# Optimization experiments

Hardware: AMD Instinct MI355X
Metric: run time of the kernel (lower is better)

Reference implementation:

```python
import jax, jax.numpy as jnp
import numpy as np

N_NODES = 100000
N_EDGES = 625000
D = 128
N_LAYERS = 10

def setup_inputs() -> dict:
    key = jax.random.key(0)
    ks = jax.random.split(key, 6)
    x = jax.random.normal(ks[0], (N_NODES, D), dtype=jnp.float32)
    edge_index = jax.random.randint(ks[1], (2, N_EDGES), 0, N_NODES, dtype=jnp.int32)
    # PyG SAGEConv params per layer: lin_l (aggregated msgs, with bias), lin_r (root, no bias)
    scale = 1.0 / np.sqrt(D)
    Wl = jax.random.normal(ks[2], (N_LAYERS, D, D), dtype=jnp.float32) * scale
    Wr = jax.random.normal(ks[3], (N_LAYERS, D, D), dtype=jnp.float32) * scale
    b = jax.random.normal(ks[4], (N_LAYERS, D), dtype=jnp.float32) * 0.01
    return {"x": x, "Wl": Wl, "Wr": Wr, "b": b, "edge_index": edge_index}

def reference(x, Wl, Wr, b, edge_index):
    src = edge_index[0]
    dst = edge_index[1]
    n = x.shape[0]
    # in-degree for mean aggregation (clamped to avoid div by zero)
    deg = jax.ops.segment_sum(jnp.ones(src.shape[0], x.dtype), dst, num_segments=n)
    deg = jnp.maximum(deg, 1.0)[:, None]
    n_layers = Wl.shape[0]
    for i in range(n_layers):
        # SAGEConv: out = lin_l(mean_{j in N(i)} x_j) + lin_r(x_i)
        agg = jax.ops.segment_sum(x[src], dst, num_segments=n) / deg
        x = agg @ Wl[i] + x @ Wr[i] + b[i]
        if i < n_layers - 1:
            x = jax.nn.relu(x)  # dropout is identity in eval mode
    return x
```

## Files before the change

kernel.cpp:

```cpp
#include <hip/hip_runtime.h>
#include <hip/hip_bf16.h>

#define N_NODES 100000
#define N_EDGES 625000
#define D 128
#define N_LAYERS 10
#define SCAN_BLOCKS 98

typedef __attribute__((ext_vector_type(8))) short bf16x8;
typedef __attribute__((ext_vector_type(4))) float floatx4;

static __device__ __forceinline__ ushort f2bf(float f) {
    uint u = __float_as_uint(f);
    u += 0x7fff + ((u >> 16) & 1);
    return (ushort)(u >> 16);
}
static __device__ __forceinline__ float bf2f(ushort h) {
    return __uint_as_float(((uint)h) << 16);
}


__global__ void hist_kernel(const int* __restrict__ dst, int* __restrict__ deg) {
    int e = blockIdx.x * blockDim.x + threadIdx.x;
    if (e < N_EDGES) atomicAdd(&deg[dst[e]], 1);
}

__global__ void scanA_kernel(const int* __restrict__ deg, int* __restrict__ offsets,
                             int* __restrict__ blockSums) {
    __shared__ int s[1024];
    int tid = threadIdx.x;
    int i = blockIdx.x * 1024 + tid;
    int v = (i < N_NODES) ? deg[i] : 0;
    s[tid] = v;
    __syncthreads();
    for (int d = 1; d < 1024; d <<= 1) {
        int t = (tid >= d) ? s[tid - d] : 0;
        __syncthreads();
        s[tid] += t;
        __syncthreads();
    }
    if (i < N_NODES) offsets[i] = s[tid] - v;
    if (tid == 1023) blockSums[blockIdx.x] = s[1023];
}

__global__ void scanB_kernel(const int* __restrict__ blockSums, int* __restrict__ blockOffsets) {
    __shared__ int s[128];
    int tid = threadIdx.x;
    int v = (tid < SCAN_BLOCKS) ? blockSums[tid] : 0;
    s[tid] = v;
    __syncthreads();
    for (int d = 1; d < 128; d <<= 1) {
        int t = (tid >= d) ? s[tid - d] : 0;
        __syncthreads();
        s[tid] += t;
        __syncthreads();
    }
    blockOffsets[tid] = s[tid] - v;
}

__global__ void scanC_kernel(int* __restrict__ offsets, const int* __restrict__ blockOffsets) {
    int i = blockIdx.x * 1024 + threadIdx.x;
    if (i < N_NODES) offsets[i] += blockOffsets[blockIdx.x];
}

__global__ void invdeg_kernel(const int* __restrict__ deg, float* __restrict__ invdeg) {
    int i = blockIdx.x * blockDim.x + threadIdx.x;
    if (i < N_NODES) {
        int d = deg[i];
        invdeg[i] = 1.0f / (float)(d > 0 ? d : 1);
    }
}

__global__ void scatter_kernel(const int* __restrict__ src, const int* __restrict__ dst,
                               const int* __restrict__ offsets, int* __restrict__ fill,
                               int* __restrict__ srcSorted) {
    int e = blockIdx.x * blockDim.x + threadIdx.x;
    if (e < N_EDGES) {
        int d_ = dst[e];
        int pos = offsets[d_] + atomicAdd(&fill[d_], 1);
        srcSorted[pos] = src[e];
    }
}

__global__ void wsplit_kernel(const float* __restrict__ Wl, const float* __restrict__ Wr,
                              ushort* __restrict__ Whi, ushort* __restrict__ Wlo) {
    int t = blockIdx.x * blockDim.x + threadIdx.x;
    if (t >= N_LAYERS * 4 * 16 * 64) return;
    int lane  = t & 63;
    int ntile = (t >> 6) & 15;
    int s     = (t >> 10) & 3;
    int layer = t >> 12;
    int n = ntile * 16 + (lane & 15);
    int kbase = s * 32 + (lane >> 4) * 8;
    const float* W = (n < 128) ? (Wl + (size_t)layer * D * D + n)
                               : (Wr + (size_t)layer * D * D + (n - 128));
    size_t off = (size_t)t * 8;
#pragma unroll
    for (int j = 0; j < 8; ++j) {
        float w = W[(size_t)(kbase + j) * D];
        ushort hh = f2bf(w);
        Whi[off + j] = hh;
        Wlo[off + j] = f2bf(w - bf2f(hh));
    }
}

__global__ __launch_bounds__(256) void gemm_hz(
        const float* __restrict__ X, const ushort* __restrict__ Whi,
        const ushort* __restrict__ Wlo, const float* __restrict__ bias,
        uint* __restrict__ h2out, float* __restrict__ z) {
    __shared__ ushort Ahi[2][4 * 64 * 8];
    __shared__ ushort Alo[2][4 * 64 * 8];

    int tid  = threadIdx.x;
    int lane = tid & 63;
    int wave = tid >> 6;

    int r    = tid >> 4;
    int t0   = tid & 15;
    int s_st = t0 >> 2;
    int q_st = t0 & 3;
    int lanep = (q_st << 4) | r;
    int stIdx = (s_st * 64 + (lanep ^ (s_st << 2))) * 8;

    int q  = lane >> 4;
    int cc = lane & 15;

    int ntileMap[4];
#pragma unroll
    for (int nt = 0; nt < 4; ++nt)
        ntileMap[nt] = (wave < 2) ? (wave * 2 + (nt & 1) + ((nt >> 1) << 2))
                                  : (wave * 4 + nt);

    float bsc[4] = {0.f, 0.f, 0.f, 0.f};
    if (wave >= 2) {
#pragma unroll
        for (int nt = 0; nt < 4; ++nt)
            bsc[nt] = bias[((wave * 4 + nt) - 8) * 16 + cc];
    }

    for (int mt = blockIdx.x; mt < N_NODES / 32; mt += gridDim.x) {
        int row0 = mt * 32;
#pragma unroll
        for (int st = 0; st < 2; ++st) {
            const float* xp = X + (size_t)(row0 + st * 16 + r) * D + t0 * 8;
            float4 v0 = *(const float4*)xp;
            float4 v1 = *(const float4*)(xp + 4);
            float a[8] = {v0.x, v0.y, v0.z, v0.w, v1.x, v1.y, v1.z, v1.w};
            ushort hi8[8], lo8[8];
#pragma unroll
            for (int j = 0; j < 8; ++j) {
                ushort hh = f2bf(a[j]);
                hi8[j] = hh;
                lo8[j] = f2bf(a[j] - bf2f(hh));
            }
            *(bf16x8*)&Ahi[st][stIdx] = *(bf16x8*)hi8;
            *(bf16x8*)&Alo[st][stIdx] = *(bf16x8*)lo8;
        }
        __syncthreads();

        floatx4 acc0[4], acc1[4];
#pragma unroll
        for (int nt = 0; nt < 4; ++nt) {
            acc0[nt] = (floatx4){0.f, 0.f, 0.f, 0.f};
            acc1[nt] = (floatx4){0.f, 0.f, 0.f, 0.f};
        }
#pragma unroll
        for (int s = 0; s < 4; ++s) {
            int aIdx = (s * 64 + (lane ^ (s << 2))) * 8;
            bf16x8 ah0 = *(const bf16x8*)&Ahi[0][aIdx];
            bf16x8 al0 = *(const bf16x8*)&Alo[0][aIdx];
            bf16x8 ah1 = *(const bf16x8*)&Ahi[1][aIdx];
            bf16x8 al1 = *(const bf16x8*)&Alo[1][aIdx];
#pragma unroll
            for (int nt = 0; nt < 4; ++nt) {
                size_t wo = ((size_t)(s * 16 + ntileMap[nt]) * 64 + lane) * 8;
                bf16x8 wh = *(const bf16x8*)&Whi[wo];
                bf16x8 wl = *(const bf16x8*)&Wlo[wo];
                acc0[nt] = __builtin_amdgcn_mfma_f32_16x16x32_bf16(ah0, wh, acc0[nt], 0, 0, 0);
                acc0[nt] = __builtin_amdgcn_mfma_f32_16x16x32_bf16(al0, wh, acc0[nt], 0, 0, 0);
                acc0[nt] = __builtin_amdgcn_mfma_f32_16x16x32_bf16(ah0, wl, acc0[nt], 0, 0, 0);
                acc1[nt] = __builtin_amdgcn_mfma_f32_16x16x32_bf16(ah1, wh, acc1[nt], 0, 0, 0);
                acc1[nt] = __builtin_amdgcn_mfma_f32_16x16x32_bf16(al1, wh, acc1[nt], 0, 0, 0);
                acc1[nt] = __builtin_amdgcn_mfma_f32_16x16x32_bf16(ah1, wl, acc1[nt], 0, 0, 0);
            }
        }
        __syncthreads();

#pragma unroll
        for (int st = 0; st < 2; ++st) {
            floatx4* acc = st ? acc1 : acc0;
            int rowb = row0 + st * 16;
            if (wave < 2) {
#pragma unroll
                for (int p = 0; p < 2; ++p) {
                    int c = wave * 32 + p * 16 + cc;
#pragma unroll
                    for (int rr = 0; rr < 4; ++rr) {
                        uint lo = f2bf(acc[p][rr]);
                        uint hi = f2bf(acc[p + 2][rr]);
                        h2out[(size_t)(rowb + q * 4 + rr) * 64 + c] = lo | (hi << 16);
                    }
                }
            } else {
#pragma unroll
                for (int nt = 0; nt < 4; ++nt) {
                    int col = ((wave * 4 + nt) - 8) * 16 + cc;
#pragma unroll
                    for (int rr = 0; rr < 4; ++rr) {
                        int row = rowb + q * 4 + rr;
                        z[(size_t)row * D + col] = acc[nt][rr] + bsc[nt];
                    }
                }
            }
        }
    }
}

__global__ __launch_bounds__(256) void agg_add_kernel(
        const uint* __restrict__ h2, const int* __restrict__ srcSorted,
        const int* __restrict__ offsets, const int* __restrict__ deg,
        const float* __restrict__ invdeg, const float* __restrict__ zin,
        float* __restrict__ out, int relu) {
    int node = blockIdx.x * 4 + (threadIdx.x >> 6);
    int lane = threadIdx.x & 63;
    int off = offsets[node];
    int cnt = deg[node];
    float sx = 0.f, sy = 0.f;
    if (cnt > 0) {
        int nv = cnt < 64 ? cnt : 64;
        int idxv = srcSorted[off + ((lane < nv) ? lane : 0)];
        for (int k = 0; k < nv; k += 8) {
            int sidx[8];
#pragma unroll
            for (int j = 0; j < 8; ++j) {
                int kk = k + j;
                sidx[j] = __shfl(idxv, (kk < nv) ? kk : 0, 64);
            }
            uint u[8];
#pragma unroll
            for (int j = 0; j < 8; ++j)
                u[j] = h2[(size_t)sidx[j] * 64 + lane];
#pragma unroll
            for (int j = 0; j < 8; ++j) {
                float m = ((k + j) < nv) ? 1.f : 0.f;
                sx += m * __uint_as_float(u[j] << 16);
                sy += m * __uint_as_float(u[j] & 0xffff0000u);
            }
        }
        for (int k = 64; k < cnt; ++k) {
            int s = srcSorted[off + k];
            uint u = h2[(size_t)s * 64 + lane];
            sx += __uint_as_float(u << 16);
            sy += __uint_as_float(u & 0xffff0000u);
        }
    }
    float inv = invdeg[node];
    float ox = sx * inv + zin[(size_t)node * 128 + lane];
    float oy = sy * inv + zin[(size_t)node * 128 + 64 + lane];
    if (relu) { ox = fmaxf(ox, 0.f); oy = fmaxf(oy, 0.f); }
    out[(size_t)node * 128 + lane] = ox;
    out[(size_t)node * 128 + 64 + lane] = oy;
}

extern "C" void kernel_launch(void* const* d_in, const int* in_sizes, int n_in,
                              void* d_out, int out_size, void* d_ws, size_t ws_size,
                              hipStream_t stream) {
    const float* x  = (const float*)d_in[0];
    const float* Wl = (const float*)d_in[1];
    const float* Wr = (const float*)d_in[2];
    const float* b  = (const float*)d_in[3];
    const int*   ei = (const int*)d_in[4];
    const int* src = ei;
    const int* dst = ei + N_EDGES;
    float* out = (float*)d_out;

    char* w = (char*)d_ws;
    auto alloc = [&](size_t bytes) -> char* {
        char* p = w;
        w += (bytes + 255) & ~(size_t)255;
        return p;
    };
    float*  zx        = (float*)alloc((size_t)N_NODES * D * 4);
    uint*   hbuf      = (uint*)alloc((size_t)N_NODES * 64 * 4);
    ushort* Whi       = (ushort*)alloc((size_t)N_LAYERS * 4 * 16 * 64 * 8 * 2);
    ushort* Wlo       = (ushort*)alloc((size_t)N_LAYERS * 4 * 16 * 64 * 8 * 2);
    int*    deg       = (int*)alloc((size_t)N_NODES * 4);
    int*    offsets   = (int*)alloc((size_t)N_NODES * 4);
    int*    fill      = (int*)alloc((size_t)N_NODES * 4);
    int*    srcSorted = (int*)alloc((size_t)N_EDGES * 4);
    int*    blockSums = (int*)alloc(128 * 4);
    int*    blockOffs = (int*)alloc(128 * 4);
    float*  invdeg    = (float*)alloc((size_t)N_NODES * 4);

    hipMemsetAsync(deg, 0, (size_t)N_NODES * 4, stream);
    hipMemsetAsync(fill, 0, (size_t)N_NODES * 4, stream);

    hist_kernel<<<(N_EDGES + 255) / 256, 256, 0, stream>>>(dst, deg);
    scanA_kernel<<<SCAN_BLOCKS, 1024, 0, stream>>>(deg, offsets, blockSums);
    scanB_kernel<<<1, 128, 0, stream>>>(blockSums, blockOffs);
    scanC_kernel<<<SCAN_BLOCKS, 1024, 0, stream>>>(offsets, blockOffs);
    invdeg_kernel<<<(N_NODES + 255) / 256, 256, 0, stream>>>(deg, invdeg);
    scatter_kernel<<<(N_EDGES + 255) / 256, 256, 0, stream>>>(src, dst, offsets, fill, srcSorted);
    wsplit_kernel<<<(N_LAYERS * 4 * 16 * 64 + 255) / 256, 256, 0, stream>>>(Wl, Wr, Whi, Wlo);

    const float* cur = x;
    for (int L = 0; L < N_LAYERS; ++L) {
        size_t woff = (size_t)L * 4 * 16 * 64 * 8;
        gemm_hz<<<N_NODES / 32, 256, 0, stream>>>(cur, Whi + woff, Wlo + woff,
                                                  b + (size_t)L * D, hbuf, zx);
        float* o = (L == N_LAYERS - 1) ? out : zx;
        agg_add_kernel<<<N_NODES / 4, 256, 0, stream>>>(
            hbuf, srcSorted, offsets, deg, invdeg, zx, o, (L < N_LAYERS - 1) ? 1 : 0);
        cur = o;
    }
}
```

Baseline: 884.4 us.

## Fuse aggregation with next layer's GEMM into a single per-layer kernel

Each middle layer now runs one kernel that gathers neighbour messages for 32 nodes, adds the root/bias term and applies ReLU, then writes the bf16 hi/lo split straight into shared memory and runs the MFMA GEMM for the next layer. This removes the fp32 activation round trip to global memory and one launch per layer, and double-buffers the packed message buffer so reads and writes do not alias. The gather path uses a shared index load per wave covering 8 nodes. The trade-off is more register and LDS pressure, and each GEMM block now waits on irregular gather latency.

```diff
diff --git a/kernel.cpp b/kernel.cpp
--- a/kernel.cpp
+++ b/kernel.cpp
@@ -63,12 +63,14 @@
     if (i < N_NODES) offsets[i] += blockOffsets[blockIdx.x];
 }
 
-__global__ void invdeg_kernel(const int* __restrict__ deg, float* __restrict__ invdeg) {
+__global__ void invdeg_kernel(const int* __restrict__ deg, float* __restrict__ invdeg,
+                              int* __restrict__ offsets) {
     int i = blockIdx.x * blockDim.x + threadIdx.x;
     if (i < N_NODES) {
         int d = deg[i];
         invdeg[i] = 1.0f / (float)(d > 0 ? d : 1);
     }
+    if (i == 0) offsets[N_NODES] = N_EDGES;
 }
 
 __global__ void scatter_kernel(const int* __restrict__ src, const int* __restrict__ dst,
@@ -138,7 +140,8 @@
             bsc[nt] = bias[((wave * 4 + nt) - 8) * 16 + cc];
     }
 
-    for (int mt = blockIdx.x; mt < N_NODES / 32; mt += gridDim.x) {
+    int mt = blockIdx.x;
+    {
         int row0 = mt * 32;
 #pragma unroll
         for (int st = 0; st < 2; ++st) {
@@ -184,7 +187,6 @@
                 acc1[nt] = __builtin_amdgcn_mfma_f32_16x16x32_bf16(ah1, wl, acc1[nt], 0, 0, 0);
             }
         }
-        __syncthreads();
 
 #pragma unroll
         for (int st = 0; st < 2; ++st) {
@@ -216,11 +218,183 @@
     }
 }
 
+__global__ __launch_bounds__(256) void fused_layer(
+        const uint* __restrict__ h2in, const int* __restrict__ srcSorted,
+        const int* __restrict__ offsets, const float* __restrict__ invdeg,
+        const float* __restrict__ zio, const ushort* __restrict__ Whi,
+        const ushort* __restrict__ Wlo, const float* __restrict__ bias,
+        uint* __restrict__ h2out) {
+    __shared__ ushort Ahi[2][4 * 64 * 8];
+    __shared__ ushort Alo[2][4 * 64 * 8];
+
+    int tid  = threadIdx.x;
+    int lane = tid & 63;
+    int wave = tid >> 6;
+    int row0 = blockIdx.x * 32;
+
+    int n0 = row0 + wave * 8;
+    int offA[9];
+#pragma unroll
+    for (int i = 0; i < 9; ++i) offA[i] = offsets[n0 + i];
+    int off0 = offA[0];
+    int total = offA[8] - off0;
+    int idxv = srcSorted[min(off0 + ((lane < total) ? lane : 0), N_EDGES - 1)];
+
+    for (int i = 0; i < 8; ++i) {
+        int sRel = offA[i] - off0;
+        int eRel = offA[i + 1] - off0;
+        int cnt = eRel - sRel;
+        float sx = 0.f, sy = 0.f;
+        if (cnt > 0 && eRel <= 64) {
+            for (int k = sRel; k < eRel; k += 8) {
+                int sidx[8];
+#pragma unroll
+                for (int j = 0; j < 8; ++j) {
+                    int kk = k + j;
+                    sidx[j] = __shfl(idxv, (kk < eRel) ? kk : sRel, 64);
+                }
+                uint u[8];
+#pragma unroll
+                for (int j = 0; j < 8; ++j)
+                    u[j] = h2in[(size_t)sidx[j] * 64 + lane];
+#pragma unroll
+                for (int j = 0; j < 8; ++j) {
+                    float m = ((k + j) < eRel) ? 1.f : 0.f;
+                    sx += m * __uint_as_float(u[j] << 16);
+                    sy += m * __uint_as_float(u[j] & 0xffff0000u);
+                }
+            }
+        } else if (cnt > 0) {
+            int offn = offA[i];
+            int nv = cnt < 64 ? cnt : 64;
+            int idxn = srcSorted[offn + ((lane < nv) ? lane : 0)];
+            for (int k = 0; k < nv; k += 8) {
+                int sidx[8];
+#pragma unroll
+                for (int j = 0; j < 8; ++j) {
+                    int kk = k + j;
+                    sidx[j] = __shfl(idxn, (kk < nv) ? kk : 0, 64);
+                }
+                uint u[8];
+#pragma unroll
+                for (int j = 0; j < 8; ++j)
+                    u[j] = h2in[(size_t)sidx[j] * 64 + lane];
+#pragma unroll
+                for (int j = 0; j < 8; ++j) {
+                    float m = ((k + j) < nv) ? 1.f : 0.f;
+                    sx += m * __uint_as_float(u[j] << 16);
+                    sy += m * __uint_as_float(u[j] & 0xffff0000u);
+                }
+            }
+            for (int k = 64; k < cnt; ++k) {
+                int s = srcSorted[offn + k];
+                uint u = h2in[(size_t)s * 64 + lane];
+                sx += __uint_as_float(u << 16);
+                sy += __uint_as_float(u & 0xffff0000u);
+            }
+        }
+        int node = n0 + i;
+        float inv = invdeg[node];
+        float ox = fmaxf(sx * inv + zio[(size_t)node * D + lane], 0.f);
+        float oy = fmaxf(sy * inv + zio[(size_t)node * D + 64 + lane], 0.f);
+
+        int local = wave * 8 + i;
+        int st = local >> 4;
+        int m = local & 15;
+        {
+            int c = lane;
+            int s_ = c >> 5, q_ = (c >> 3) & 3, j_ = c & 7;
+            int elem = (s_ * 64 + (((q_ << 4) | m) ^ (s_ << 2))) * 8 + j_;
+            ushort hh = f2bf(ox);
+            Ahi[st][elem] = hh;
+            Alo[st][elem] = f2bf(ox - bf2f(hh));
+        }
+        {
+            int c = lane + 64;
+            int s_ = c >> 5, q_ = (c >> 3) & 3, j_ = c & 7;
+            int elem = (s_ * 64 + (((q_ << 4) | m) ^ (s_ << 2))) * 8 + j_;
+            ushort hh = f2bf(oy);
+            Ahi[st][elem] = hh;
+            Alo[st][elem] = f2bf(oy - bf2f(hh));
+        }
+    }
+    __syncthreads();
+
+    int q  = lane >> 4;
+    int cc = lane & 15;
+    int ntileMap[4];
+#pragma unroll
+    for (int nt = 0; nt < 4; ++nt)
+        ntileMap[nt] = (wave < 2) ? (wave * 2 + (nt & 1) + ((nt >> 1) << 2))
+                                  : (wave * 4 + nt);
+    float bsc[4] = {0.f, 0.f, 0.f, 0.f};
+    if (wave >= 2) {
+#pragma unroll
+        for (int nt = 0; nt < 4; ++nt)
+            bsc[nt] = bias[((wave * 4 + nt) - 8) * 16 + cc];
+    }
+
+    floatx4 acc0[4], acc1[4];
+#pragma unroll
+    for (int nt = 0; nt < 4; ++nt) {
+        acc0[nt] = (floatx4){0.f, 0.f, 0.f, 0.f};
+        acc1[nt] = (floatx4){0.f, 0.f, 0.f, 0.f};
+    }
+#pragma unroll
+    for (int s = 0; s < 4; ++s) {
+        int aIdx = (s * 64 + (lane ^ (s << 2))) * 8;
+        bf16x8 ah0 = *(const bf16x8*)&Ahi[0][aIdx];
+        bf16x8 al0 = *(const bf16x8*)&Alo[0][aIdx];
+        bf16x8 ah1 = *(const bf16x8*)&Ahi[1][aIdx];
+        bf16x8 al1 = *(const bf16x8*)&Alo[1][aIdx];
+#pragma unroll
+        for (int nt = 0; nt < 4; ++nt) {
+            size_t wo = ((size_t)(s * 16 + ntileMap[nt]) * 64 + lane) * 8;
+            bf16x8 wh = *(const bf16x8*)&Whi[wo];
+            bf16x8 wl = *(const bf16x8*)&Wlo[wo];
+            acc0[nt] = __builtin_amdgcn_mfma_f32_16x16x32_bf16(ah0, wh, acc0[nt], 0, 0, 0);
+            acc0[nt] = __builtin_amdgcn_mfma_f32_16x16x32_bf16(al0, wh, acc0[nt], 0, 0, 0);
+            acc0[nt] = __builtin_amdgcn_mfma_f32_16x16x32_bf16(ah0, wl, acc0[nt], 0, 0, 0);
+            acc1[nt] = __builtin_amdgcn_mfma_f32_16x16x32_bf16(ah1, wh, acc1[nt], 0, 0, 0);
+            acc1[nt] = __builtin_amdgcn_mfma_f32_16x16x32_bf16(al1, wh, acc1[nt], 0, 0, 0);
+            acc1[nt] = __builtin_amdgcn_mfma_f32_16x16x32_bf16(ah1, wl, acc1[nt], 0, 0, 0);
+        }
+    }
+
+#pragma unroll
+    for (int st = 0; st < 2; ++st) {
+        floatx4* acc = st ? acc1 : acc0;
+        int rowb = row0 + st * 16;
+        if (wave < 2) {
+#pragma unroll
+            for (int p = 0; p < 2; ++p) {
+                int c = wave * 32 + p * 16 + cc;
+#pragma unroll
+                for (int rr = 0; rr < 4; ++rr) {
+                    uint lo = f2bf(acc[p][rr]);
+                    uint hi = f2bf(acc[p + 2][rr]);
+                    h2out[(size_t)(rowb + q * 4 + rr) * 64 + c] = lo | (hi << 16);
+                }
+            }
+        } else {
+#pragma unroll
+            for (int nt = 0; nt < 4; ++nt) {
+                int col = ((wave * 4 + nt) - 8) * 16 + cc;
+#pragma unroll
+                for (int rr = 0; rr < 4; ++rr) {
+                    int row = rowb + q * 4 + rr;
+                    ((float*)zio)[(size_t)row * D + col] = acc[nt][rr] + bsc[nt];
+                }
+            }
+        }
+    }
+}
+
 __global__ __launch_bounds__(256) void agg_add_kernel(
         const uint* __restrict__ h2, const int* __restrict__ srcSorted,
         const int* __restrict__ offsets, const int* __restrict__ deg,
         const float* __restrict__ invdeg, const float* __restrict__ zin,
-        float* __restrict__ out, int relu) {
+        float* __restrict__ out) {
     int node = blockIdx.x * 4 + (threadIdx.x >> 6);
     int lane = threadIdx.x & 63;
     int off = offsets[node];
@@ -255,11 +429,8 @@
         }
     }
     float inv = invdeg[node];
-    float ox = sx * inv + zin[(size_t)node * 128 + lane];
-    float oy = sy * inv + zin[(size_t)node * 128 + 64 + lane];
-    if (relu) { ox = fmaxf(ox, 0.f); oy = fmaxf(oy, 0.f); }
-    out[(size_t)node * 128 + lane] = ox;
-    out[(size_t)node * 128 + 64 + lane] = oy;
+    out[(size_t)node * 128 + lane] = sx * inv + zin[(size_t)node * 128 + lane];
+    out[(size_t)node * 128 + 64 + lane] = sy * inv + zin[(size_t)node * 128 + 64 + lane];
 }
 
 extern "C" void kernel_launch(void* const* d_in, const int* in_sizes, int n_in,
@@ -281,11 +452,12 @@
         return p;
     };
     float*  zx        = (float*)alloc((size_t)N_NODES * D * 4);
-    uint*   hbuf      = (uint*)alloc((size_t)N_NODES * 64 * 4);
+    uint*   hbufA     = (uint*)alloc((size_t)N_NODES * 64 * 4);
+    uint*   hbufB     = (uint*)alloc((size_t)N_NODES * 64 * 4);
     ushort* Whi       = (ushort*)alloc((size_t)N_LAYERS * 4 * 16 * 64 * 8 * 2);
     ushort* Wlo       = (ushort*)alloc((size_t)N_LAYERS * 4 * 16 * 64 * 8 * 2);
     int*    deg       = (int*)alloc((size_t)N_NODES * 4);
-    int*    offsets   = (int*)alloc((size_t)N_NODES * 4);
+    int*    offsets   = (int*)alloc((size_t)(N_NODES + 1) * 4);
     int*    fill      = (int*)alloc((size_t)N_NODES * 4);
     int*    srcSorted = (int*)alloc((size_t)N_EDGES * 4);
     int*    blockSums = (int*)alloc(128 * 4);
@@ -299,18 +471,20 @@
     scanA_kernel<<<SCAN_BLOCKS, 1024, 0, stream>>>(deg, offsets, blockSums);
     scanB_kernel<<<1, 128, 0, stream>>>(blockSums, blockOffs);
     scanC_kernel<<<SCAN_BLOCKS, 1024, 0, stream>>>(offsets, blockOffs);
-    invdeg_kernel<<<(N_NODES + 255) / 256, 256, 0, stream>>>(deg, invdeg);
+    invdeg_kernel<<<(N_NODES + 255) / 256, 256, 0, stream>>>(deg, invdeg, offsets);
     scatter_kernel<<<(N_EDGES + 255) / 256, 256, 0, stream>>>(src, dst, offsets, fill, srcSorted);
     wsplit_kernel<<<(N_LAYERS * 4 * 16 * 64 + 255) / 256, 256, 0, stream>>>(Wl, Wr, Whi, Wlo);
 
-    const float* cur = x;
-    for (int L = 0; L < N_LAYERS; ++L) {
+    gemm_hz<<<N_NODES / 32, 256, 0, stream>>>(x, Whi, Wlo, b, hbufA, zx);
+    uint* hin = hbufA;
+    uint* hout = hbufB;
+    for (int L = 1; L < N_LAYERS; ++L) {
         size_t woff = (size_t)L * 4 * 16 * 64 * 8;
-        gemm_hz<<<N_NODES / 32, 256, 0, stream>>>(cur, Whi + woff, Wlo + woff,
-                                                  b + (size_t)L * D, hbuf, zx);
-        float* o = (L == N_LAYERS - 1) ? out : zx;
-        agg_add_kernel<<<N_NODES / 4, 256, 0, stream>>>(
-            hbuf, srcSorted, offsets, deg, invdeg, zx, o, (L < N_LAYERS - 1) ? 1 : 0);
-        cur = o;
-    }
-}
+        fused_layer<<<N_NODES / 32, 256, 0, stream>>>(
+            hin, srcSorted, offsets, invdeg, zx,
+            Whi + woff, Wlo + woff, b + (size_t)L * D, hout);
+        uint* t = hin; hin = hout; hout = t;
+    }
+    agg_add_kernel<<<N_NODES / 4, 256, 0, stream>>>(
+        hin, srcSorted, offsets, deg, invdeg, zx, out);
+}
```

Measured after the change: 823.9 us. 1.07x faster.
